# Kernel optimization log

Measured on AMD Instinct MI355X. Metric: run time of the kernel, lower is better.

Reference implementation:

```python
import jax, jax.numpy as jnp
import numpy as np

N, E, D, DH, MH, MO = 100000, 1600000, 128, 512, 512, 128
EPS_BN = 1e-5
EPS_LN = 1e-5


def setup_inputs() -> dict:
    key = jax.random.key(0)
    ks = jax.random.split(key, 16)
    def lin(k, fan_in, shape):
        return jax.random.normal(k, shape, jnp.float32) / np.sqrt(fan_in)
    return {
        'x': jax.random.normal(ks[0], (N, D), jnp.float32),
        'src': jax.random.randint(ks[1], (E,), 0, N, jnp.int32),
        'dst': jax.random.randint(ks[2], (E,), 0, N, jnp.int32),
        'gcn_w': lin(ks[3], D, (D, D)),
        'gcn_b': jnp.zeros((D,), jnp.float32),
        'ff_w1': lin(ks[4], D, (D, DH)),
        'ff_b1': jnp.zeros((DH,), jnp.float32),
        'ln_g': jnp.ones((DH,), jnp.float32),
        'ln_b': jnp.zeros((DH,), jnp.float32),
        'ff_w2': lin(ks[5], DH, (DH, D)),
        'ff_b2': jnp.zeros((D,), jnp.float32),
        'fc1_w': lin(ks[6], D, (D, MH)),
        'fc1_b': jnp.zeros((MH,), jnp.float32),
        'bn1_g': jnp.ones((MH,), jnp.float32),
        'bn1_b': jnp.zeros((MH,), jnp.float32),
        'fc2_w': lin(ks[7], MH, (MH, MH)),
        'fc2_b': jnp.zeros((MH,), jnp.float32),
        'bn2_g': jnp.ones((MH,), jnp.float32),
        'bn2_b': jnp.zeros((MH,), jnp.float32),
        'fc3_w': lin(ks[8], MH, (MH, MO)),
        'fc3_b': jnp.zeros((MO,), jnp.float32),
        'bn3_g': jnp.ones((MO,), jnp.float32),
        'bn3_b': jnp.zeros((MO,), jnp.float32),
        'fc4_w': lin(ks[9], MO, (MO, 1)),
        'fc4_b': jnp.zeros((1,), jnp.float32),
    }


def _gelu(x):
    return jax.nn.gelu(x, approximate=False)  # torch nn.GELU default (erf)


def _batchnorm(x, g, b):
    # BatchNorm1d in training mode: batch statistics, biased variance
    m = jnp.mean(x, axis=0)
    v = jnp.var(x, axis=0)
    return (x - m) * jax.lax.rsqrt(v + EPS_BN) * g + b


def reference(x, src, dst, gcn_w, gcn_b, ff_w1, ff_b1, ln_g, ln_b, ff_w2, ff_b2,
              fc1_w, fc1_b, bn1_g, bn1_b, fc2_w, fc2_b, bn2_g, bn2_b,
              fc3_w, fc3_b, bn3_g, bn3_b, fc4_w, fc4_b):
    n = x.shape[0]
    ones = jnp.ones(src.shape[0], x.dtype)
    out_deg = jnp.clip(jax.ops.segment_sum(ones, src, num_segments=n), 1.0)
    in_deg = jnp.clip(jax.ops.segment_sum(ones, dst, num_segments=n), 1.0)
    # GraphConv, norm='both': left-normalize, aggregate, matmul (in==out), right-normalize, bias
    h = x * (out_deg ** -0.5)[:, None]
    agg = jax.ops.segment_sum(h[src], dst, num_segments=n)  # [N, D]
    h = agg @ gcn_w
    h = h * (in_deg ** -0.5)[:, None] + gcn_b
    # FeedForwardLayer: lin1 -> GELU -> LayerNorm -> lin2
    f = _gelu(h @ ff_w1 + ff_b1)
    mu = jnp.mean(f, axis=-1, keepdims=True)
    var = jnp.var(f, axis=-1, keepdims=True)
    f = (f - mu) * jax.lax.rsqrt(var + EPS_LN) * ln_g + ln_b
    h = f @ ff_w2 + ff_b2  # [N, D]
    # MLP head
    h = _batchnorm(_gelu(h @ fc1_w + fc1_b), bn1_g, bn1_b)
    h = _batchnorm(_gelu(h @ fc2_w + fc2_b), bn2_g, bn2_b)
    h = _batchnorm(_gelu(h @ fc3_w + fc3_b), bn3_g, bn3_b)
    return h @ fc4_w + fc4_b  # [N, 1]
```

## Files before the change

kernel.cpp:

```cpp
#include <hip/hip_runtime.h>
#include <hip/hip_bf16.h>

#define N_NODES 100000
#define NPAD    100096
#define NRB     782
#define E_EDGES 1600000
#define NBLK_SCAN 98

#define HNR  4
#define HP   64
#define HCHK 25000
#define HRSZ 32768

#define NBK  196
#define PCHK 6250

#define AS1 __attribute__((address_space(1)))
#define AS3 __attribute__((address_space(3)))

typedef unsigned int   uint;
typedef unsigned short ushort;
typedef __attribute__((ext_vector_type(8))) short bfx8;
typedef __attribute__((ext_vector_type(4))) float fx4;

__device__ __forceinline__ float bf2f(ushort u) {
    return __uint_as_float(((uint)u) << 16);
}
__device__ __forceinline__ ushort f2bf(float f) {
    uint x = __float_as_uint(f);
    return (ushort)((x + 0x7FFFu + ((x >> 16) & 1u)) >> 16);
}
__device__ __forceinline__ float gelu_fast(float x) {
    float u = 1.5957691f * __builtin_fmaf(0.044715f * x * x, x, x);
    return x / (1.0f + __expf(-u));
}
__device__ __forceinline__ float wave_sum(float v) {
    #pragma unroll
    for (int m = 1; m < 64; m <<= 1) v += __shfl_xor(v, m, 64);
    return v;
}
__device__ __forceinline__ int xcd_swz(int orig, int nwg) {
    int q = nwg >> 3, r = nwg & 7;
    int x = orig & 7, o = orig >> 3;
    return (x < r ? x * (q + 1) : r * (q + 1) + (x - r) * q) + o;
}

__global__ void k_hist(const int* __restrict__ idx, uint* __restrict__ part)
{
    __shared__ uint h[HRSZ / 2];
    int c = blockIdx.x & (HP - 1);
    int r = blockIdx.x / HP;
    int t = threadIdx.x;
    for (int i = t; i < HRSZ / 2; i += 256) h[i] = 0u;
    __syncthreads();
    int base = r << 15;
    int e0 = c * HCHK;
    for (int e = e0 + t; e < e0 + HCHK; e += 256) {
        int v = idx[e] - base;
        if ((uint)v < (uint)HRSZ)
            atomicAdd(&h[v >> 1], 1u << ((v & 1) * 16));
    }
    __syncthreads();
    uint* dst = part + ((size_t)blockIdx.x << 14);
    for (int i = t; i < HRSZ / 2; i += 256) dst[i] = h[i];
}

__global__ void k_degmerge(const uint* __restrict__ partO, const uint* __restrict__ partI,
                           int* __restrict__ inc, float* __restrict__ oscale,
                           float* __restrict__ ininv)
{
    int n = blockIdx.x * 256 + threadIdx.x;
    if (n >= NPAD) return;
    int r = n >> 15, i = (n & 32767) >> 1, hi = (n & 1) * 16;
    const uint* po = partO + ((size_t)(r * HP) << 14) + i;
    const uint* pi = partI + ((size_t)(r * HP) << 14) + i;
    uint so = 0, si = 0;
    for (int c = 0; c < HP; ++c) {
        so += (po[(size_t)c << 14] >> hi) & 0xffffu;
        si += (pi[(size_t)c << 14] >> hi) & 0xffffu;
    }
    inc[n] = (int)si;
    oscale[n] = rsqrtf((float)max((int)so, 1));
    ininv[n] = rsqrtf((float)max((int)si, 1));
}

__global__ void k_scan1(const int* __restrict__ inc, int* __restrict__ coff, int* __restrict__ btot)
{
    __shared__ int a[1024], bsh[1024];
    int t = threadIdx.x;
    int i = blockIdx.x * 1024 + t;
    a[t] = (i < N_NODES) ? inc[i] : 0;
    __syncthreads();
    int* s = a; int* d = bsh;
    for (int dd = 1; dd < 1024; dd <<= 1) {
        int v = s[t] + ((t >= dd) ? s[t - dd] : 0);
        d[t] = v;
        __syncthreads();
        int* tmp = s; s = d; d = tmp;
    }
    if (i < N_NODES) coff[i + 1] = s[t];
    if (t == 1023) btot[blockIdx.x] = s[t];
}

__global__ void k_scan2(int* __restrict__ btot)
{
    __shared__ int a[128], bsh[128];
    int t = threadIdx.x;
    a[t] = (t < NBLK_SCAN) ? btot[t] : 0;
    __syncthreads();
    int* s = a; int* d = bsh;
    for (int dd = 1; dd < 128; dd <<= 1) {
        int v = s[t] + ((t >= dd) ? s[t - dd] : 0);
        d[t] = v;
        __syncthreads();
        int* tmp = s; s = d; d = tmp;
    }
    if (t < NBLK_SCAN) btot[t] = s[t];
}

__global__ void k_scan3(int* __restrict__ coff, const int* __restrict__ btot)
{
    int i = blockIdx.x * 256 + threadIdx.x;
    if (i == 0) coff[0] = 0;
    if (i < N_NODES) {
        int blk = i >> 10;
        if (blk > 0) coff[i + 1] += btot[blk - 1];
    }
}

__global__ void k_curinit(const int* __restrict__ coff, int* __restrict__ gcur)
{
    int t = threadIdx.x;
    if (t < NBK) gcur[t] = coff[t << 9];
}

__global__ __launch_bounds__(256) void k_part(const int* __restrict__ src, const int* __restrict__ dst,
                                              int* __restrict__ gcur, uint* __restrict__ tmp)
{
    __shared__ int cnt[NBK], rcnt[NBK], base[NBK], loff[NBK];
    __shared__ int sa[256], sb[256];
    __shared__ uint arr[PCHK];
    int t = threadIdx.x;
    if (t < NBK) { cnt[t] = 0; rcnt[t] = 0; }
    __syncthreads();
    int e0 = blockIdx.x * PCHK;
    for (int e = e0 + t; e < e0 + PCHK; e += 256)
        atomicAdd(&cnt[dst[e] >> 9], 1);
    __syncthreads();
    sa[t] = (t < NBK) ? cnt[t] : 0;
    __syncthreads();
    int* s = sa; int* d = sb;
    for (int dd = 1; dd < 256; dd <<= 1) {
        int v = s[t] + ((t >= dd) ? s[t - dd] : 0);
        d[t] = v;
        __syncthreads();
        int* w = s; s = d; d = w;
    }
    if (t < NBK) {
        loff[t] = s[t] - cnt[t];
        base[t] = atomicAdd(&gcur[t], cnt[t]);
    }
    __syncthreads();
    for (int e = e0 + t; e < e0 + PCHK; e += 256) {
        int dv = dst[e];
        int b = dv >> 9;
        int r = atomicAdd(&rcnt[b], 1);
        arr[loff[b] + r] = ((uint)src[e] << 9) | (uint)(dv & 511);
    }
    __syncthreads();
    for (int b = 0; b < NBK; ++b) {
        int n = cnt[b], lo = loff[b], gb = base[b];
        for (int i = t; i < n; i += 256)
            tmp[gb + i] = arr[lo + i];
    }
}

__global__ __launch_bounds__(256) void k_fill2(const uint* __restrict__ tmp, const int* __restrict__ coff,
                                               int* __restrict__ eidx)
{
    __shared__ int lco[512];
    __shared__ int lcnt[512];
    int b = blockIdx.x, t = threadIdx.x;
    int n0 = b << 9;
    for (int i = t; i < 512; i += 256) {
        int node = n0 + i;
        lco[i] = (node <= N_NODES) ? coff[node] : E_EDGES;
        lcnt[i] = 0;
    }
    __syncthreads();
    int s0 = coff[n0];
    int s1 = (n0 + 512 <= N_NODES) ? coff[n0 + 512] : E_EDGES;
    for (int e = s0 + t; e < s1; e += 256) {
        uint v = tmp[e];
        int dl = v & 511;
        int r = atomicAdd(&lcnt[dl], 1);
        eidx[lco[dl] + r] = (int)(v >> 9);
    }
}

__global__ void k_xhat(const float* __restrict__ x, const float* __restrict__ oscale,
                       ushort* __restrict__ xh)
{
    size_t i = (size_t)blockIdx.x * 256 + threadIdx.x;
    size_t e0 = i * 4;
    int row = (int)(e0 >> 7);
    uint2 o;
    if (row < N_NODES) {
        float4 v = *(const float4*)(x + e0);
        float s = oscale[row];
        o.x = (uint)f2bf(v.x * s) | ((uint)f2bf(v.y * s) << 16);
        o.y = (uint)f2bf(v.z * s) | ((uint)f2bf(v.w * s) << 16);
    } else {
        o.x = 0u; o.y = 0u;
    }
    *(uint2*)(xh + e0) = o;
}

__global__ void k_agg(const int* __restrict__ off, const int* __restrict__ eidx,
                      const ushort* __restrict__ xh, ushort* __restrict__ agg)
{
    int wid = threadIdx.x >> 6, lane = threadIdx.x & 63;
    int r = blockIdx.x * 4 + wid;
    if (r >= NPAD) return;
    int f = lane & 15;
    int g = lane >> 4;
    float a[8] = {0.f, 0.f, 0.f, 0.f, 0.f, 0.f, 0.f, 0.f};
    if (r < N_NODES) {
        int s = off[r], e = off[r + 1];
        for (int i = s + g; i < e; i += 4) {
            int sv = eidx[i];
            bfx8 v = *(const bfx8*)(xh + (size_t)sv * 128 + f * 8);
            #pragma unroll
            for (int k = 0; k < 8; ++k) a[k] += bf2f((ushort)v[k]);
        }
    }
    #pragma unroll
    for (int k = 0; k < 8; ++k) {
        a[k] += __shfl_xor(a[k], 16, 64);
        a[k] += __shfl_xor(a[k], 32, 64);
    }
    if (g == 0) {
        bfx8 o;
        #pragma unroll
        for (int k = 0; k < 8; ++k) o[k] = (short)f2bf(a[k]);
        *(bfx8*)(agg + (size_t)r * 128 + f * 8) = o;
    }
}

__global__ void k_wT(const float* __restrict__ W, int K, int M, ushort* __restrict__ Wt)
{
    int id = blockIdx.x * 256 + threadIdx.x;
    if (id < K * M) {
        int m = id / K, k = id - m * K;
        Wt[id] = f2bf(W[(size_t)k * M + m]);
    }
}

__global__ void k_wT_ln(const float* __restrict__ W, const float* __restrict__ g,
                        const float* __restrict__ b, const float* __restrict__ b2,
                        ushort* __restrict__ Wt, float* __restrict__ u, float* __restrict__ t)
{
    int wid = threadIdx.x >> 6, lane = threadIdx.x & 63;
    int m = blockIdx.x * 4 + wid;
    if (m >= 128) return;
    float us = 0.f, ts = 0.f;
    for (int k = lane; k < 512; k += 64) {
        float w = W[(size_t)k * 128 + m];
        float gk = g[k], bk = b[k];
        Wt[(size_t)m * 512 + k] = f2bf(gk * w);
        us += gk * w; ts += bk * w;
    }
    us = wave_sum(us); ts = wave_sum(ts);
    if (lane == 0) { u[m] = us; t[m] = ts + b2[m]; }
}

template <int K1, int EPI1, int STATS2>
__global__ __launch_bounds__(512, 4) void k_fused(
    const ushort* __restrict__ A1, const ushort* __restrict__ B1t,
    const ushort* __restrict__ B2t, ushort* __restrict__ C,
    const float* __restrict__ c1v0, const float* __restrict__ r1v0,
    const float* __restrict__ r1v1, const float* __restrict__ c1v1,
    const float* __restrict__ bias2,
    float* __restrict__ lnS, float* __restrict__ lnC,
    float* __restrict__ pS, float* __restrict__ pQ)
{
    __shared__ __align__(16) char smem[32768 + 32768 + 2048];
    char* A2 = smem;
    char* S  = smem + 32768;
    float* st_s = (float*)(smem + 65536);
    float* st_q = (float*)(smem + 65536 + 1024);

    const int rb = xcd_swz(blockIdx.x, gridDim.x);
    const int tid = threadIdx.x;
    const int lane = tid & 63;
    const int wid = tid >> 6;
    const int wr = wid >> 2;
    const int wc = wid & 3;
    const int m0 = wr * 64;
    const int n0 = wc * 32;
    const int frl = lane & 15;
    const int kg = lane >> 4;

    char* As = S;
    char* Bs = S + 16384;
    fx4 acc[4][2] = {};
    const ushort* Arow0 = A1 + (size_t)(rb * 128) * K1;

    for (int kb = 0; kb < K1; kb += 64) {
        #pragma unroll
        for (int c = 0; c < 2; ++c) {
            int b = c * 8192 + tid * 16;
            int row = b >> 7;
            int cibs = (b & 127) ^ ((row & 7) << 4);
            const char* ga = (const char*)(Arow0 + (size_t)row * K1 + kb) + cibs;
            const char* gb = (const char*)(B1t + (size_t)row * K1 + kb) + cibs;
            char* la = As + c * 8192 + (wid << 10);
            char* lb = Bs + c * 8192 + (wid << 10);
            __builtin_amdgcn_global_load_lds((const AS1 void*)ga, (AS3 void*)la, 16, 0, 0);
            __builtin_amdgcn_global_load_lds((const AS1 void*)gb, (AS3 void*)lb, 16, 0, 0);
        }
        __syncthreads();
        #pragma unroll
        for (int kk = 0; kk < 2; ++kk) {
            bfx8 av[4], bv[2];
            #pragma unroll
            for (int i = 0; i < 4; ++i) {
                int ar = m0 + i * 16 + frl;
                av[i] = *(const bfx8*)(As + ((ar * 128 + kk * 64 + kg * 16) ^ ((ar & 7) << 4)));
            }
            #pragma unroll
            for (int j = 0; j < 2; ++j) {
                int br = n0 + j * 16 + frl;
                bv[j] = *(const bfx8*)(Bs + ((br * 128 + kk * 64 + kg * 16) ^ ((br & 7) << 4)));
            }
            #pragma unroll
            for (int i = 0; i < 4; ++i)
                #pragma unroll
                for (int j = 0; j < 2; ++j)
                    acc[i][j] = __builtin_amdgcn_mfma_f32_16x16x32_bf16(av[i], bv[j], acc[i][j], 0, 0, 0);
        }
        __syncthreads();
    }

    #pragma unroll
    for (int j = 0; j < 2; ++j) {
        int colL = n0 + j * 16 + frl;
        float c0 = c1v0[colL];
        float c1 = (EPI1 == 3) ? c1v1[colL] : 0.f;
        #pragma unroll
        for (int i = 0; i < 4; ++i) {
            #pragma unroll
            for (int r = 0; r < 4; ++r) {
                int rowL = m0 + i * 16 + kg * 4 + r;
                int grow = rb * 128 + rowL;
                float v = acc[i][j][r];
                if (EPI1 == 0) v = v * r1v0[grow] + c0;
                else           v = r1v0[grow] * v + r1v1[grow] * c1 + c0;
                *(ushort*)(A2 + rowL * 256 + ((colL * 2) ^ ((rowL & 7) << 4))) = f2bf(v);
            }
        }
    }
    __syncthreads();

    float rs = 0.f, rq = 0.f;
    const int rowR = tid >> 2;
    const int qR = tid & 3;

    for (int cb2 = 0; cb2 < 4; ++cb2) {
        #pragma unroll
        for (int c = 0; c < 4; ++c) {
            int b = c * 8192 + tid * 16;
            int row = b >> 8;
            int cibs = (b & 255) ^ ((row & 7) << 4);
            const char* gb = (const char*)(B2t + (size_t)(cb2 * 128 + row) * 128) + cibs;
            char* lb = S + c * 8192 + (wid << 10);
            __builtin_amdgcn_global_load_lds((const AS1 void*)gb, (AS3 void*)lb, 16, 0, 0);
        }
        __syncthreads();

        fx4 a2[4][2] = {};
        #pragma unroll
        for (int kk = 0; kk < 4; ++kk) {
            int c2 = kk * 64 + kg * 16;
            bfx8 av[4], bv[2];
            #pragma unroll
            for (int i = 0; i < 4; ++i) {
                int ar = m0 + i * 16 + frl;
                av[i] = *(const bfx8*)(A2 + ar * 256 + (c2 ^ ((ar & 7) << 4)));
            }
            #pragma unroll
            for (int j = 0; j < 2; ++j) {
                int br = n0 + j * 16 + frl;
                bv[j] = *(const bfx8*)(S + br * 256 + (c2 ^ ((br & 7) << 4)));
            }
            #pragma unroll
            for (int i = 0; i < 4; ++i)
                #pragma unroll
                for (int j = 0; j < 2; ++j)
                    a2[i][j] = __builtin_amdgcn_mfma_f32_16x16x32_bf16(av[i], bv[j], a2[i][j], 0, 0, 0);
        }
        __syncthreads();

        #pragma unroll
        for (int j = 0; j < 2; ++j) {
            int colL = n0 + j * 16 + frl;
            float bcol = bias2[cb2 * 128 + colL];
            float sL = 0.f, qL = 0.f;
            #pragma unroll
            for (int i = 0; i < 4; ++i) {
                #pragma unroll
                for (int r = 0; r < 4; ++r) {
                    float v = gelu_fast(a2[i][j][r] + bcol);
                    int rowL = m0 + i * 16 + kg * 4 + r;
                    if (STATS2 == 1) {
                        if (rb * 128 + rowL < N_NODES) { sL += v; qL += v * v; }
                    }
                    *(ushort*)(S + rowL * 256 + ((colL * 2) ^ ((rowL & 7) << 4))) = f2bf(v);
                }
            }
            if (STATS2 == 1) {
                sL += __shfl_xor(sL, 16, 64); sL += __shfl_xor(sL, 32, 64);
                qL += __shfl_xor(qL, 16, 64); qL += __shfl_xor(qL, 32, 64);
                if (kg == 0) {
                    st_s[wr * 128 + colL] = sL;
                    st_q[wr * 128 + colL] = qL;
                }
            }
        }
        __syncthreads();

        {
            int r2 = tid >> 4;
            int s2 = tid & 15;
            #pragma unroll
            for (int pass = 0; pass < 4; ++pass) {
                int rowL = pass * 32 + r2;
                int boff = rowL * 256 + ((s2 * 16) ^ ((rowL & 7) << 4));
                bfx8 v = *(const bfx8*)(S + boff);
                *(bfx8*)((char*)(C + (size_t)(rb * 128 + rowL) * 512 + cb2 * 128) + s2 * 16) = v;
            }
        }
        if (STATS2 == 1 && tid < 128) {
            size_t pidx = ((size_t)rb * 4 + cb2) * 128 + tid;
            pS[pidx] = st_s[tid] + st_s[128 + tid];
            pQ[pidx] = st_q[tid] + st_q[128 + tid];
        }
        if (STATS2 == 2) {
            #pragma unroll
            for (int ss = 0; ss < 4; ++ss) {
                int boff = rowR * 256 + (((qR * 64 + ss * 16)) ^ ((rowR & 7) << 4));
                bfx8 v = *(const bfx8*)(S + boff);
                #pragma unroll
                for (int k2 = 0; k2 < 8; ++k2) {
                    float f = bf2f((ushort)v[k2]);
                    rs += f; rq += f * f;
                }
            }
        }
        __syncthreads();
    }

    if (STATS2 == 2) {
        rs += __shfl_xor(rs, 1, 64); rs += __shfl_xor(rs, 2, 64);
        rq += __shfl_xor(rq, 1, 64); rq += __shfl_xor(rq, 2, 64);
        if (qR == 0) {
            float mean = rs * (1.f / 512.f);
            float var = fmaxf(rq * (1.f / 512.f) - mean * mean, 0.f);
            float sr = rsqrtf(var + 1e-5f);
            int grow = rb * 128 + rowR;
            lnS[grow] = sr;
            lnC[grow] = -mean * sr;
        }
    }
}

template <int EPI, int STATS>
__global__ __launch_bounds__(256, 4) void k_gemm(
    const ushort* __restrict__ A, const ushort* __restrict__ Bt,
    ushort* __restrict__ C, int K, int M,
    const float* __restrict__ colv0, const float* __restrict__ rowv0,
    float* __restrict__ pS, float* __restrict__ pQ, int grb0)
{
    __shared__ __align__(16) char smem[32768 + (STATS == 1 ? 1024 : 0)];
    char* AsB = smem;
    char* BsB = smem + 16384;

    const int nwg = gridDim.x;
    const int wgid = xcd_swz(blockIdx.x, nwg);
    const int nCB = M >> 7;
    const int cb = wgid % nCB;
    const int rb = wgid / nCB;
    const int tid = threadIdx.x;
    const int lane = tid & 63;
    const int wid = tid >> 6;
    const int m0 = (wid >> 1) * 64;
    const int n0 = (wid & 1) * 64;
    const int frl = lane & 15;
    const int kg = lane >> 4;

    float* statsf = (float*)(smem + 32768);
    if (STATS == 1 && tid < 128) { statsf[tid] = 0.f; statsf[128 + tid] = 0.f; }

    fx4 acc[4][4] = {};

    const ushort* Arow0 = A + (size_t)(rb * 128) * K;
    const ushort* Brow0 = Bt + (size_t)(cb * 128) * K;

    for (int kb = 0; kb < K; kb += 64) {
        #pragma unroll
        for (int c = 0; c < 4; ++c) {
            int b = c * 4096 + tid * 16;
            int row = b >> 7;
            int cibs = (b & 127) ^ ((row & 7) << 4);
            const char* ga = (const char*)(Arow0 + (size_t)row * K + kb) + cibs;
            const char* gb = (const char*)(Brow0 + (size_t)row * K + kb) + cibs;
            char* la = AsB + c * 4096 + (wid << 10);
            char* lb = BsB + c * 4096 + (wid << 10);
            __builtin_amdgcn_global_load_lds((const AS1 void*)ga, (AS3 void*)la, 16, 0, 0);
            __builtin_amdgcn_global_load_lds((const AS1 void*)gb, (AS3 void*)lb, 16, 0, 0);
        }
        __syncthreads();
        #pragma unroll
        for (int kk = 0; kk < 2; ++kk) {
            bfx8 av[4], bv[4];
            #pragma unroll
            for (int i = 0; i < 4; ++i) {
                int ar = m0 + i * 16 + frl;
                int ab = (ar * 128 + kk * 64 + kg * 16) ^ ((ar & 7) << 4);
                av[i] = *(const bfx8*)(AsB + ab);
                int br = n0 + i * 16 + frl;
                int bb = (br * 128 + kk * 64 + kg * 16) ^ ((br & 7) << 4);
                bv[i] = *(const bfx8*)(BsB + bb);
            }
            #pragma unroll
            for (int i = 0; i < 4; ++i)
                #pragma unroll
                for (int j = 0; j < 4; ++j)
                    acc[i][j] = __builtin_amdgcn_mfma_f32_16x16x32_bf16(av[i], bv[j], acc[i][j], 0, 0, 0);
        }
        __syncthreads();
    }

    float sL[4] = {0.f, 0.f, 0.f, 0.f}, qL[4] = {0.f, 0.f, 0.f, 0.f};
    #pragma unroll
    for (int j = 0; j < 4; ++j) {
        int colL = n0 + j * 16 + frl;
        float c0 = colv0[cb * 128 + colL];
        #pragma unroll
        for (int i = 0; i < 4; ++i) {
            int rbaseL = m0 + i * 16 + kg * 4;
            #pragma unroll
            for (int r = 0; r < 4; ++r) {
                float v = acc[i][j][r];
                int rowL = rbaseL + r;
                int grow = (grb0 + rb) * 128 + rowL;
                if (EPI == 0) v = v * rowv0[grow] + c0;
                else          v = gelu_fast(v + c0);
                if (STATS == 1) {
                    if (grow < N_NODES) { sL[j] += v; qL[j] += v * v; }
                }
                int boff = rowL * 256 + ((colL * 2) ^ ((rowL & 7) << 4));
                *(ushort*)(smem + boff) = f2bf(v);
            }
        }
    }
    if (STATS == 1) {
        #pragma unroll
        for (int j = 0; j < 4; ++j) {
            float s = sL[j], q = qL[j];
            s += __shfl_xor(s, 16, 64); s += __shfl_xor(s, 32, 64);
            q += __shfl_xor(q, 16, 64); q += __shfl_xor(q, 32, 64);
            if (kg == 0) {
                atomicAdd(&statsf[n0 + j * 16 + frl], s);
                atomicAdd(&statsf[128 + n0 + j * 16 + frl], q);
            }
        }
    }
    __syncthreads();
    {
        int r2 = tid >> 4;
        int s2 = tid & 15;
        #pragma unroll
        for (int pass = 0; pass < 8; ++pass) {
            int rowL = pass * 16 + r2;
            int boff = rowL * 256 + ((s2 * 16) ^ ((rowL & 7) << 4));
            bfx8 v = *(const bfx8*)(smem + boff);
            *(bfx8*)((char*)(C + (size_t)(rb * 128 + rowL) * M + cb * 128) + s2 * 16) = v;
        }
    }
    if (STATS == 1 && tid < 128) {
        size_t pidx = ((size_t)(grb0 + rb) * nCB + cb) * 128 + tid;
        pS[pidx] = statsf[tid];
        pQ[pidx] = statsf[128 + tid];
    }
}

__global__ void k_colmerge(const float* __restrict__ pS, const float* __restrict__ pQ,
                           float* __restrict__ oS, float* __restrict__ oQ, int M)
{
    int wid = threadIdx.x >> 6, lane = threadIdx.x & 63;
    int m = blockIdx.x * 4 + wid;
    if (m >= M) return;
    int nCB = M >> 7, cb = m >> 7, colL = m & 127;
    float s = 0.f, q = 0.f;
    for (int rb = lane; rb < NRB; rb += 64) {
        size_t idx = ((size_t)rb * nCB + cb) * 128 + colL;
        s += pS[idx]; q += pQ[idx];
    }
    s = wave_sum(s); q = wave_sum(q);
    if (lane == 0) { oS[m] = s; oQ[m] = q; }
}

__global__ void k_fold(const float* __restrict__ W, const float* __restrict__ bw,
                       const float* __restrict__ g, const float* __restrict__ bb,
                       const float* __restrict__ sum, const float* __restrict__ sqs,
                       int K, int M, ushort* __restrict__ WtO, float* __restrict__ bO)
{
    int wid = threadIdx.x >> 6, lane = threadIdx.x & 63;
    int m = blockIdx.x * 4 + wid;
    if (m >= M) return;
    float acc = 0.f;
    for (int k = lane; k < K; k += 64) {
        float mean = sum[k] * (1.f / (float)N_NODES);
        float var = sqs[k] * (1.f / (float)N_NODES) - mean * mean;
        float s = g[k] * rsqrtf(var + 1e-5f);
        float t = bb[k] - mean * s;
        float w = W[(size_t)k * M + m];
        WtO[(size_t)m * K + k] = f2bf(w * s);
        acc += t * w;
    }
    acc = wave_sum(acc);
    if (lane == 0) bO[m] = bw[m] + acc;
}

__global__ void k_out(const ushort* __restrict__ m3, const ushort* __restrict__ w4,
                      const float* __restrict__ b4, float* __restrict__ out)
{
    int wid = threadIdx.x >> 6, lane = threadIdx.x & 63;
    int r = blockIdx.x * 4 + wid;
    if (r >= N_NODES) return;
    uint u = *(const uint*)(m3 + (size_t)r * 128 + lane * 2);
    uint w = *(const uint*)(w4 + lane * 2);
    float acc = bf2f((ushort)(u & 0xffffu)) * bf2f((ushort)(w & 0xffffu))
              + bf2f((ushort)(u >> 16)) * bf2f((ushort)(w >> 16));
    acc = wave_sum(acc);
    if (lane == 0) out[r] = acc + b4[0];
}

extern "C" void kernel_launch(void* const* d_in, const int* in_sizes, int n_in,
                              void* d_out, int out_size, void* d_ws, size_t ws_size,
                              hipStream_t stream)
{
    const float* x     = (const float*)d_in[0];
    const int*   src   = (const int*)d_in[1];
    const int*   dst   = (const int*)d_in[2];
    const float* gcn_w = (const float*)d_in[3];
    const float* gcn_b = (const float*)d_in[4];
    const float* ff_w1 = (const float*)d_in[5];
    const float* ff_b1 = (const float*)d_in[6];
    const float* ln_g  = (const float*)d_in[7];
    const float* ln_b  = (const float*)d_in[8];
    const float* ff_w2 = (const float*)d_in[9];
    const float* ff_b2 = (const float*)d_in[10];
    const float* fc1_w = (const float*)d_in[11];
    const float* fc1_b = (const float*)d_in[12];
    const float* bn1_g = (const float*)d_in[13];
    const float* bn1_b = (const float*)d_in[14];
    const float* fc2_w = (const float*)d_in[15];
    const float* fc2_b = (const float*)d_in[16];
    const float* bn2_g = (const float*)d_in[17];
    const float* bn2_b = (const float*)d_in[18];
    const float* fc3_w = (const float*)d_in[19];
    const float* fc3_b = (const float*)d_in[20];
    const float* bn3_g = (const float*)d_in[21];
    const float* bn3_b = (const float*)d_in[22];
    const float* fc4_w = (const float*)d_in[23];
    const float* fc4_b = (const float*)d_in[24];
    float* out = (float*)d_out;
    (void)in_sizes; (void)n_in; (void)out_size;

    char* base = (char*)d_ws;
    char* p = base;
    auto alloc = [&](size_t bytes) -> char* {
        char* r = p;
        p += (bytes + 255) & ~(size_t)255;
        return r;
    };
    int*    inc    = (int*)alloc((size_t)NPAD * 4);
    int*    coff   = (int*)alloc(((size_t)NPAD + 1) * 4);
    int*    btot   = (int*)alloc(128 * 4);
    int*    gcur   = (int*)alloc(256 * 4);
    int*    eidx   = (int*)alloc((size_t)E_EDGES * 4);
    float*  oscale = (float*)alloc((size_t)NPAD * 4);
    float*  ininv  = (float*)alloc((size_t)NPAD * 4);
    float*  bns    = (float*)alloc(6 * 512 * 4);
    float*  b2p    = (float*)alloc(512 * 4);
    float*  b3p    = (float*)alloc(128 * 4);
    float*  b4p    = (float*)alloc(4);
    float*  lnS    = (float*)alloc((size_t)NPAD * 4);
    float*  lnC    = (float*)alloc((size_t)NPAD * 4);
    float*  lnU    = (float*)alloc(128 * 4);
    float*  lnT    = (float*)alloc(128 * 4);
    float*  pS     = (float*)alloc((size_t)4 * NPAD * 4);
    float*  pQ     = (float*)alloc((size_t)4 * NPAD * 4);
    ushort* gwT    = (ushort*)alloc(128 * 128 * 2);
    ushort* ff1T   = (ushort*)alloc(512 * 128 * 2);
    ushort* ff2T   = (ushort*)alloc(128 * 512 * 2);
    ushort* fc1T   = (ushort*)alloc(512 * 128 * 2);
    ushort* fc2T   = (ushort*)alloc(512 * 512 * 2);
    ushort* fc3T   = (ushort*)alloc(128 * 512 * 2);
    ushort* w4t    = (ushort*)alloc(128 * 2);
    ushort* buf1   = (ushort*)alloc((size_t)NPAD * 128 * 2);
    ushort* bufC   = (ushort*)alloc((size_t)NPAD * 512 * 2);

    size_t used = (size_t)(p - base);
    bool   sep  = (used + (size_t)NPAD * 512 * 2) <= ws_size;
    ushort* m2  = sep ? (ushort*)alloc((size_t)NPAD * 512 * 2) : bufC;

    uint* partO = (uint*)bufC;
    uint* partI = partO + (size_t)HNR * HP * (HRSZ / 2);
    uint* etmp  = (uint*)bufC;
    ushort* xh  = bufC;
    ushort* agg = buf1;

    float* bn1s = bns;
    float* bn1q = bns + 512;
    float* bn2s = bns + 1024;
    float* bn2q = bns + 1536;
    float* bn3s = bns + 2048;
    float* bn3q = bns + 2560;

    k_hist<<<HNR * HP, 256, 0, stream>>>(src, partO);
    k_hist<<<HNR * HP, 256, 0, stream>>>(dst, partI);
    k_degmerge<<<(NPAD + 255) / 256, 256, 0, stream>>>(partO, partI, inc, oscale, ininv);
    k_scan1<<<NBLK_SCAN, 1024, 0, stream>>>(inc, coff, btot);
    k_scan2<<<1, 128, 0, stream>>>(btot);
    k_scan3<<<(N_NODES + 255) / 256, 256, 0, stream>>>(coff, btot);
    k_curinit<<<1, 256, 0, stream>>>(coff, gcur);
    k_part<<<E_EDGES / PCHK, 256, 0, stream>>>(src, dst, gcur, etmp);
    k_fill2<<<NBK, 256, 0, stream>>>(etmp, coff, eidx);
    k_xhat<<<(NPAD / 256) * 32, 256, 0, stream>>>(x, oscale, xh);
    k_agg<<<NPAD / 4, 256, 0, stream>>>(coff, eidx, xh, agg);

    k_wT<<<(128 * 128) / 256, 256, 0, stream>>>(gcn_w, 128, 128, gwT);
    k_wT<<<(128 * 512) / 256, 256, 0, stream>>>(ff_w1, 128, 512, ff1T);
    k_wT<<<(128 * 512) / 256, 256, 0, stream>>>(fc1_w, 128, 512, fc1T);
    k_wT_ln<<<32, 256, 0, stream>>>(ff_w2, ln_g, ln_b, ff_b2, ff2T, lnU, lnT);

    k_fused<128, 0, 2><<<NRB, 512, 0, stream>>>(agg, gwT, ff1T, bufC,
                                                gcn_b, ininv, nullptr, nullptr, ff_b1,
                                                lnS, lnC, nullptr, nullptr);
    k_fused<512, 3, 1><<<NRB, 512, 0, stream>>>(bufC, ff2T, fc1T, bufC,
                                                lnT, lnS, lnC, lnU, fc1_b,
                                                nullptr, nullptr, pS, pQ);
    k_colmerge<<<128, 256, 0, stream>>>(pS, pQ, bn1s, bn1q, 512);
    k_fold<<<512 / 4, 256, 0, stream>>>(fc2_w, fc2_b, bn1_g, bn1_b, bn1s, bn1q, 512, 512, fc2T, b2p);
    if (sep) {
        k_gemm<1, 1><<<4 * NRB, 256, 0, stream>>>(bufC, fc2T, m2, 512, 512,
                                                  b2p, nullptr, pS, pQ, 0);
    } else {
        const int cOff[6] = {0, 195, 390, 585, 780, 782};
        for (int c = 0; c < 5; ++c) {
            int rb0 = cOff[c], nrb = cOff[c + 1] - rb0;
            k_gemm<1, 1><<<nrb * 4, 256, 0, stream>>>(bufC + (size_t)rb0 * 128 * 512, fc2T,
                                                      buf1, 512, 512,
                                                      b2p, nullptr, pS, pQ, rb0);
            hipMemcpyAsync(bufC + (size_t)rb0 * 128 * 512, buf1,
                           (size_t)nrb * 128 * 512 * 2, hipMemcpyDeviceToDevice, stream);
        }
    }
    k_colmerge<<<128, 256, 0, stream>>>(pS, pQ, bn2s, bn2q, 512);
    k_fold<<<128 / 4, 256, 0, stream>>>(fc3_w, fc3_b, bn2_g, bn2_b, bn2s, bn2q, 512, 128, fc3T, b3p);
    k_gemm<1, 1><<<NRB, 256, 0, stream>>>(m2, fc3T, buf1, 512, 128,
                                          b3p, nullptr, pS, pQ, 0);
    k_colmerge<<<32, 256, 0, stream>>>(pS, pQ, bn3s, bn3q, 128);
    k_fold<<<1, 256, 0, stream>>>(fc4_w, fc4_b, bn3_g, bn3_b, bn3s, bn3q, 128, 1, w4t, b4p);
    k_out<<<N_NODES / 4, 256, 0, stream>>>(buf1, w4t, b4p, out);
}
```

Measured before the change: 655.6 us.

## Merge small prep kernels and widen GEMM blocks to 512 threads

```diff
diff --git a/kernel.cpp b/kernel.cpp
--- a/kernel.cpp
+++ b/kernel.cpp
@@ -32,7 +32,7 @@
 }
 __device__ __forceinline__ float gelu_fast(float x) {
     float u = 1.5957691f * __builtin_fmaf(0.044715f * x * x, x, x);
-    return x / (1.0f + __expf(-u));
+    return x * __builtin_amdgcn_rcpf(1.0f + __expf(-u));
 }
 __device__ __forceinline__ float wave_sum(float v) {
     #pragma unroll
@@ -45,11 +45,16 @@
     return (x < r ? x * (q + 1) : r * (q + 1) + (x - r) * q) + o;
 }
 
-__global__ void k_hist(const int* __restrict__ idx, uint* __restrict__ part)
+__global__ void k_hist2(const int* __restrict__ src, const int* __restrict__ dst,
+                        uint* __restrict__ partO, uint* __restrict__ partI)
 {
     __shared__ uint h[HRSZ / 2];
-    int c = blockIdx.x & (HP - 1);
-    int r = blockIdx.x / HP;
+    int half = blockIdx.x >> 8;
+    int bb = blockIdx.x & 255;
+    const int* idx = half ? dst : src;
+    uint* part = half ? partI : partO;
+    int c = bb & (HP - 1);
+    int r = bb / HP;
     int t = threadIdx.x;
     for (int i = t; i < HRSZ / 2; i += 256) h[i] = 0u;
     __syncthreads();
@@ -61,8 +66,8 @@
             atomicAdd(&h[v >> 1], 1u << ((v & 1) * 16));
     }
     __syncthreads();
-    uint* dst = part + ((size_t)blockIdx.x << 14);
-    for (int i = t; i < HRSZ / 2; i += 256) dst[i] = h[i];
+    uint* dstp = part + ((size_t)bb << 14);
+    for (int i = t; i < HRSZ / 2; i += 256) dstp[i] = h[i];
 }
 
 __global__ void k_degmerge(const uint* __restrict__ partO, const uint* __restrict__ partI,
@@ -118,20 +123,21 @@
     if (t < NBLK_SCAN) btot[t] = s[t];
 }
 
-__global__ void k_scan3(int* __restrict__ coff, const int* __restrict__ btot)
+__global__ void k_scan3(int* __restrict__ coff, const int* __restrict__ btot,
+                        int* __restrict__ gcur)
 {
     int i = blockIdx.x * 256 + threadIdx.x;
-    if (i == 0) coff[0] = 0;
+    if (i == 0) { coff[0] = 0; gcur[0] = 0; }
     if (i < N_NODES) {
         int blk = i >> 10;
-        if (blk > 0) coff[i + 1] += btot[blk - 1];
-    }
-}
-
-__global__ void k_curinit(const int* __restrict__ coff, int* __restrict__ gcur)
-{
-    int t = threadIdx.x;
-    if (t < NBK) gcur[t] = coff[t << 9];
+        int v = coff[i + 1];
+        if (blk > 0) v += btot[blk - 1];
+        coff[i + 1] = v;
+        if (((i + 1) & 511) == 0) {
+            int t = (i + 1) >> 9;
+            if (t < NBK) gcur[t] = v;
+        }
+    }
 }
 
 __global__ __launch_bounds__(256) void k_part(const int* __restrict__ src, const int* __restrict__ dst,
@@ -247,31 +253,35 @@
     }
 }
 
-__global__ void k_wT(const float* __restrict__ W, int K, int M, ushort* __restrict__ Wt)
-{
-    int id = blockIdx.x * 256 + threadIdx.x;
-    if (id < K * M) {
+__global__ void k_wprep(const float* __restrict__ gcn_w, const float* __restrict__ ff_w1,
+                        const float* __restrict__ fc1_w, const float* __restrict__ ff_w2,
+                        const float* __restrict__ ln_g, const float* __restrict__ ln_b,
+                        const float* __restrict__ ff_b2,
+                        ushort* __restrict__ gwT, ushort* __restrict__ ff1T,
+                        ushort* __restrict__ fc1T, ushort* __restrict__ ff2T,
+                        float* __restrict__ lnU, float* __restrict__ lnT)
+{
+    int bid = blockIdx.x, tid = threadIdx.x;
+    if (bid < 576) {
+        const float* W; ushort* Wt; int K, M, id;
+        if (bid < 64)       { W = gcn_w; Wt = gwT;  K = 128; M = 128; id = bid * 256 + tid; }
+        else if (bid < 320) { W = ff_w1; Wt = ff1T; K = 128; M = 512; id = (bid - 64) * 256 + tid; }
+        else                { W = fc1_w; Wt = fc1T; K = 128; M = 512; id = (bid - 320) * 256 + tid; }
         int m = id / K, k = id - m * K;
         Wt[id] = f2bf(W[(size_t)k * M + m]);
-    }
-}
-
-__global__ void k_wT_ln(const float* __restrict__ W, const float* __restrict__ g,
-                        const float* __restrict__ b, const float* __restrict__ b2,
-                        ushort* __restrict__ Wt, float* __restrict__ u, float* __restrict__ t)
-{
-    int wid = threadIdx.x >> 6, lane = threadIdx.x & 63;
-    int m = blockIdx.x * 4 + wid;
-    if (m >= 128) return;
-    float us = 0.f, ts = 0.f;
-    for (int k = lane; k < 512; k += 64) {
-        float w = W[(size_t)k * 128 + m];
-        float gk = g[k], bk = b[k];
-        Wt[(size_t)m * 512 + k] = f2bf(gk * w);
-        us += gk * w; ts += bk * w;
-    }
-    us = wave_sum(us); ts = wave_sum(ts);
-    if (lane == 0) { u[m] = us; t[m] = ts + b2[m]; }
+    } else {
+        int wid = tid >> 6, lane = tid & 63;
+        int m = (bid - 576) * 4 + wid;
+        float us = 0.f, ts = 0.f;
+        for (int k = lane; k < 512; k += 64) {
+            float w = ff_w2[(size_t)k * 128 + m];
+            float gk = ln_g[k], bk = ln_b[k];
+            ff2T[(size_t)m * 512 + k] = f2bf(gk * w);
+            us += gk * w; ts += bk * w;
+        }
+        us = wave_sum(us); ts = wave_sum(ts);
+        if (lane == 0) { lnU[m] = us; lnT[m] = ts + ff_b2[m]; }
+    }
 }
 
 template <int K1, int EPI1, int STATS2>
@@ -475,15 +485,17 @@
 }
 
 template <int EPI, int STATS>
-__global__ __launch_bounds__(256, 4) void k_gemm(
+__global__ __launch_bounds__(512, 4) void k_gemm(
     const ushort* __restrict__ A, const ushort* __restrict__ Bt,
     ushort* __restrict__ C, int K, int M,
     const float* __restrict__ colv0, const float* __restrict__ rowv0,
     float* __restrict__ pS, float* __restrict__ pQ, int grb0)
 {
-    __shared__ __align__(16) char smem[32768 + (STATS == 1 ? 1024 : 0)];
+    __shared__ __align__(16) char smem[32768 + (STATS == 1 ? 2048 : 0)];
     char* AsB = smem;
     char* BsB = smem + 16384;
+    float* st_s = (float*)(smem + 32768);
+    float* st_q = (float*)(smem + 32768 + 1024);
 
     const int nwg = gridDim.x;
     const int wgid = xcd_swz(blockIdx.x, nwg);
@@ -493,86 +505,80 @@
     const int tid = threadIdx.x;
     const int lane = tid & 63;
     const int wid = tid >> 6;
-    const int m0 = (wid >> 1) * 64;
-    const int n0 = (wid & 1) * 64;
+    const int wr = wid >> 2;
+    const int wc = wid & 3;
+    const int m0 = wr * 64;
+    const int n0 = wc * 32;
     const int frl = lane & 15;
     const int kg = lane >> 4;
 
-    float* statsf = (float*)(smem + 32768);
-    if (STATS == 1 && tid < 128) { statsf[tid] = 0.f; statsf[128 + tid] = 0.f; }
-
-    fx4 acc[4][4] = {};
+    fx4 acc[4][2] = {};
 
     const ushort* Arow0 = A + (size_t)(rb * 128) * K;
     const ushort* Brow0 = Bt + (size_t)(cb * 128) * K;
 
     for (int kb = 0; kb < K; kb += 64) {
         #pragma unroll
-        for (int c = 0; c < 4; ++c) {
-            int b = c * 4096 + tid * 16;
+        for (int c = 0; c < 2; ++c) {
+            int b = c * 8192 + tid * 16;
             int row = b >> 7;
             int cibs = (b & 127) ^ ((row & 7) << 4);
             const char* ga = (const char*)(Arow0 + (size_t)row * K + kb) + cibs;
             const char* gb = (const char*)(Brow0 + (size_t)row * K + kb) + cibs;
-            char* la = AsB + c * 4096 + (wid << 10);
-            char* lb = BsB + c * 4096 + (wid << 10);
+            char* la = AsB + c * 8192 + (wid << 10);
+            char* lb = BsB + c * 8192 + (wid << 10);
             __builtin_amdgcn_global_load_lds((const AS1 void*)ga, (AS3 void*)la, 16, 0, 0);
             __builtin_amdgcn_global_load_lds((const AS1 void*)gb, (AS3 void*)lb, 16, 0, 0);
         }
         __syncthreads();
         #pragma unroll
         for (int kk = 0; kk < 2; ++kk) {
-            bfx8 av[4], bv[4];
+            bfx8 av[4], bv[2];
             #pragma unroll
             for (int i = 0; i < 4; ++i) {
                 int ar = m0 + i * 16 + frl;
-                int ab = (ar * 128 + kk * 64 + kg * 16) ^ ((ar & 7) << 4);
-                av[i] = *(const bfx8*)(AsB + ab);
-                int br = n0 + i * 16 + frl;
-                int bb = (br * 128 + kk * 64 + kg * 16) ^ ((br & 7) << 4);
-                bv[i] = *(const bfx8*)(BsB + bb);
+                av[i] = *(const bfx8*)(AsB + ((ar * 128 + kk * 64 + kg * 16) ^ ((ar & 7) << 4)));
+            }
+            #pragma unroll
+            for (int j = 0; j < 2; ++j) {
+                int br = n0 + j * 16 + frl;
+                bv[j] = *(const bfx8*)(BsB + ((br * 128 + kk * 64 + kg * 16) ^ ((br & 7) << 4)));
             }
             #pragma unroll
             for (int i = 0; i < 4; ++i)
                 #pragma unroll
-                for (int j = 0; j < 4; ++j)
+                for (int j = 0; j < 2; ++j)
                     acc[i][j] = __builtin_amdgcn_mfma_f32_16x16x32_bf16(av[i], bv[j], acc[i][j], 0, 0, 0);
         }
         __syncthreads();
     }
 
-    float sL[4] = {0.f, 0.f, 0.f, 0.f}, qL[4] = {0.f, 0.f, 0.f, 0.f};
     #pragma unroll
-    for (int j = 0; j < 4; ++j) {
+    for (int j = 0; j < 2; ++j) {
         int colL = n0 + j * 16 + frl;
         float c0 = colv0[cb * 128 + colL];
+        float sL = 0.f, qL = 0.f;
         #pragma unroll
         for (int i = 0; i < 4; ++i) {
-            int rbaseL = m0 + i * 16 + kg * 4;
             #pragma unroll
             for (int r = 0; r < 4; ++r) {
                 float v = acc[i][j][r];
-                int rowL = rbaseL + r;
+                int rowL = m0 + i * 16 + kg * 4 + r;
                 int grow = (grb0 + rb) * 128 + rowL;
                 if (EPI == 0) v = v * rowv0[grow] + c0;
                 else          v = gelu_fast(v + c0);
                 if (STATS == 1) {
-                    if (grow < N_NODES) { sL[j] += v; qL[j] += v * v; }
+                    if (grow < N_NODES) { sL += v; qL += v * v; }
                 }
-                int boff = rowL * 256 + ((colL * 2) ^ ((rowL & 7) << 4));
-                *(ushort*)(smem + boff) = f2bf(v);
-            }
-        }
-    }
-    if (STATS == 1) {
-        #pragma unroll
-        for (int j = 0; j < 4; ++j) {
-            float s = sL[j], q = qL[j];
-            s += __shfl_xor(s, 16, 64); s += __shfl_xor(s, 32, 64);
-            q += __shfl_xor(q, 16, 64); q += __shfl_xor(q, 32, 64);
+                *(ushort*)(smem + rowL * 256 + ((colL * 2) ^ ((rowL & 7) << 4))) = f2bf(v);
+            }
+        }
+        if (STATS == 1) {
+            sL += __shfl_xor(sL, 16, 64); sL += __shfl_xor(sL, 32, 64);
+            qL += __shfl_xor(qL, 16, 64); qL += __shfl_xor(qL, 32, 64);
             if (kg == 0) {
-                atomicAdd(&statsf[n0 + j * 16 + frl], s);
-                atomicAdd(&statsf[128 + n0 + j * 16 + frl], q);
+                st_s[wr * 128 + colL] = sL;
+                st_q[wr * 128 + colL] = qL;
             }
         }
     }
@@ -581,8 +587,8 @@
         int r2 = tid >> 4;
         int s2 = tid & 15;
         #pragma unroll
-        for (int pass = 0; pass < 8; ++pass) {
-            int rowL = pass * 16 + r2;
+        for (int pass = 0; pass < 4; ++pass) {
+            int rowL = pass * 32 + r2;
             int boff = rowL * 256 + ((s2 * 16) ^ ((rowL & 7) << 4));
             bfx8 v = *(const bfx8*)(smem + boff);
             *(bfx8*)((char*)(C + (size_t)(rb * 128 + rowL) * M + cb * 128) + s2 * 16) = v;
@@ -590,8 +596,8 @@
     }
     if (STATS == 1 && tid < 128) {
         size_t pidx = ((size_t)(grb0 + rb) * nCB + cb) * 128 + tid;
-        pS[pidx] = statsf[tid];
-        pQ[pidx] = statsf[128 + tid];
+        pS[pidx] = st_s[tid] + st_s[128 + tid];
+        pQ[pidx] = st_q[tid] + st_q[128 + tid];
     }
 }
 
@@ -730,22 +736,18 @@
     float* bn3s = bns + 2048;
     float* bn3q = bns + 2560;
 
-    k_hist<<<HNR * HP, 256, 0, stream>>>(src, partO);
-    k_hist<<<HNR * HP, 256, 0, stream>>>(dst, partI);
+    k_hist2<<<2 * HNR * HP, 256, 0, stream>>>(src, dst, partO, partI);
     k_degmerge<<<(NPAD + 255) / 256, 256, 0, stream>>>(partO, partI, inc, oscale, ininv);
     k_scan1<<<NBLK_SCAN, 1024, 0, stream>>>(inc, coff, btot);
     k_scan2<<<1, 128, 0, stream>>>(btot);
-    k_scan3<<<(N_NODES + 255) / 256, 256, 0, stream>>>(coff, btot);
-    k_curinit<<<1, 256, 0, stream>>>(coff, gcur);
+    k_scan3<<<(N_NODES + 255) / 256, 256, 0, stream>>>(coff, btot, gcur);
     k_part<<<E_EDGES / PCHK, 256, 0, stream>>>(src, dst, gcur, etmp);
     k_fill2<<<NBK, 256, 0, stream>>>(etmp, coff, eidx);
     k_xhat<<<(NPAD / 256) * 32, 256, 0, stream>>>(x, oscale, xh);
     k_agg<<<NPAD / 4, 256, 0, stream>>>(coff, eidx, xh, agg);
 
-    k_wT<<<(128 * 128) / 256, 256, 0, stream>>>(gcn_w, 128, 128, gwT);
-    k_wT<<<(128 * 512) / 256, 256, 0, stream>>>(ff_w1, 128, 512, ff1T);
-    k_wT<<<(128 * 512) / 256, 256, 0, stream>>>(fc1_w, 128, 512, fc1T);
-    k_wT_ln<<<32, 256, 0, stream>>>(ff_w2, ln_g, ln_b, ff_b2, ff2T, lnU, lnT);
+    k_wprep<<<608, 256, 0, stream>>>(gcn_w, ff_w1, fc1_w, ff_w2, ln_g, ln_b, ff_b2,
+                                     gwT, ff1T, fc1T, ff2T, lnU, lnT);
 
     k_fused<128, 0, 2><<<NRB, 512, 0, stream>>>(agg, gwT, ff1T, bufC,
                                                 gcn_b, ininv, nullptr, nullptr, ff_b1,
@@ -756,13 +758,13 @@
     k_colmerge<<<128, 256, 0, stream>>>(pS, pQ, bn1s, bn1q, 512);
     k_fold<<<512 / 4, 256, 0, stream>>>(fc2_w, fc2_b, bn1_g, bn1_b, bn1s, bn1q, 512, 512, fc2T, b2p);
     if (sep) {
-        k_gemm<1, 1><<<4 * NRB, 256, 0, stream>>>(bufC, fc2T, m2, 512, 512,
+        k_gemm<1, 1><<<4 * NRB, 512, 0, stream>>>(bufC, fc2T, m2, 512, 512,
                                                   b2p, nullptr, pS, pQ, 0);
     } else {
         const int cOff[6] = {0, 195, 390, 585, 780, 782};
         for (int c = 0; c < 5; ++c) {
             int rb0 = cOff[c], nrb = cOff[c + 1] - rb0;
-            k_gemm<1, 1><<<nrb * 4, 256, 0, stream>>>(bufC + (size_t)rb0 * 128 * 512, fc2T,
+            k_gemm<1, 1><<<nrb * 4, 512, 0, stream>>>(bufC + (size_t)rb0 * 128 * 512, fc2T,
                                                       buf1, 512, 512,
                                                       b2p, nullptr, pS, pQ, rb0);
             hipMemcpyAsync(bufC + (size_t)rb0 * 128 * 512, buf1,
@@ -771,7 +773,7 @@
     }
     k_colmerge<<<128, 256, 0, stream>>>(pS, pQ, bn2s, bn2q, 512);
     k_fold<<<128 / 4, 256, 0, stream>>>(fc3_w, fc3_b, bn2_g, bn2_b, bn2s, bn2q, 512, 128, fc3T, b3p);
-    k_gemm<1, 1><<<NRB, 256, 0, stream>>>(m2, fc3T, buf1, 512, 128,
+    k_gemm<1, 1><<<NRB, 512, 0, stream>>>(m2, fc3T, buf1, 512, 128,
                                           b3p, nullptr, pS, pQ, 0);
     k_colmerge<<<32, 256, 0, stream>>>(pS, pQ, bn3s, bn3q, 128);
     k_fold<<<1, 256, 0, stream>>>(fc4_w, fc4_b, bn3_g, bn3_b, bn3s, bn3q, 128, 1, w4t, b4p);
```

Measured after the change: 571.9 us. -12.8%, faster.
